# Performance work log

Measured on AMD Instinct MI355X. Metric: run time of the kernel, lower is better.

The kernel has to match this reference:

```python
import jax, jax.numpy as jnp
import numpy as np

B, N, M, U, L = 2048, 256, 128, 512, 2   # batch, memory locations, memory width, num_units, num_layers
RH, WH, SH = 2, 2, 1                      # read heads, write heads, conv_shift_range
CLIP = 20.0
HEAD_R = M + 3 + (2 * SH + 1)             # 134 = k(M)+beta+g+s(2r+1)+gamma
HEAD_W = HEAD_R + 2 * M                   # 390 = + erase(M) + add(M)


def setup_inputs():
    key = jax.random.key(0)
    ks = jax.random.split(key, 12)
    def nrm(k, shape, s=0.05):
        return jax.random.normal(k, shape, jnp.float32) * s
    return {
        "X": jax.random.normal(ks[0], (B, U), jnp.float32),
        "m0": nrm(ks[1], (1, N, M), 0.5),
        "H0": nrm(ks[2], (L, 1, U)),
        "C0": nrm(ks[3], (L, 1, U)),
        "R0": nrm(ks[4], (RH, 1, M)),
        "A0": nrm(ks[5], (RH + WH, 1, N)),
        "W_prep": nrm(ks[6], (M * RH, U)),
        "b_prep": jnp.zeros((U,), jnp.float32),
        "W_lstm": nrm(ks[7], (L, 3 * U, 4 * U)),
        "b_lstm": jnp.zeros((L, 4 * U), jnp.float32),
        "W_r": nrm(ks[8], (U, RH * HEAD_R)),
        "b_r": jnp.zeros((RH * HEAD_R,), jnp.float32),
        "W_w": nrm(ks[9], (U, WH * HEAD_W)),
        "b_w": jnp.zeros((WH * HEAD_W,), jnp.float32),
        "W_ou": nrm(ks[10], (U + RH * M, U)),
        "b_ou": jnp.zeros((U,), jnp.float32),
    }


def _addressing(k, beta, g, s, gamma, m, a_prev):
    # k [B,M], beta/g/gamma [B], s [B,2*SH+1], m [B,N,M], a_prev [B,N]
    inner = jnp.einsum('bnm,bm->bn', m, k)
    k_norm = jnp.sqrt(jnp.sum(k * k, axis=1, keepdims=True))   # [B,1]
    m_norm = jnp.sqrt(jnp.sum(m * m, axis=2))                  # [B,N]
    K = inner / (k_norm * m_norm + 1e-8)
    w_c = jax.nn.softmax(beta[:, None] * K, axis=1)            # exp/sum in source == softmax
    w_g = g[:, None] * w_c + (1.0 - g[:, None]) * a_prev
    # The stacked-slice s_matrix in the source is exactly circular convolution:
    # w_conv[i] = sum_d s_d * w_g[(i - d) mod N], d in {0..SH, -SH..-1} matching s layout.
    shifts = list(range(0, SH + 1)) + list(range(-SH, 0))
    w_conv = sum(s[:, j:j + 1] * jnp.roll(w_g, shifts[j], axis=1) for j in range(2 * SH + 1))
    w_sharp = w_conv ** gamma[:, None]
    return w_sharp / jnp.sum(w_sharp, axis=1, keepdims=True)


def reference(X, m0, H0, C0, R0, A0, W_prep, b_prep, W_lstm, b_lstm,
              W_r, b_r, W_w, b_w, W_ou, b_ou):
    b = X.shape[0]
    m = jnp.broadcast_to(m0, (b, N, M))
    R_prev = [jnp.broadcast_to(jnp.tanh(R0[i]), (b, M)) for i in range(RH)]
    A_prev = [jnp.broadcast_to(jax.nn.softmax(A0[i], axis=-1), (b, N)) for i in range(RH + WH)]

    # controller
    h = jnp.concatenate(R_prev, axis=1) @ W_prep + b_prep
    for l in range(L):
        x_in = jnp.concatenate([X, h], axis=1)                              # [B,2U]
        h_prev = jnp.broadcast_to(H0[l], (b, U))
        c_prev = jnp.broadcast_to(C0[l], (b, U))
        z = jnp.concatenate([x_in, h_prev], axis=1) @ W_lstm[l] + b_lstm[l]  # [B,4U]
        i_g, f_g, g_g, o_g = jnp.split(z, 4, axis=1)
        c = jax.nn.sigmoid(f_g) * c_prev + jax.nn.sigmoid(i_g) * jnp.tanh(g_g)
        h = jax.nn.sigmoid(o_g) * jnp.tanh(c)
    h = jnp.clip(h, -CLIP, CLIP)

    r_heads = (h @ W_r + b_r).reshape(b, RH, HEAD_R)
    w_heads = (h @ W_w + b_w).reshape(b, WH, HEAD_W)
    heads = [r_heads[:, i] for i in range(RH)] + [w_heads[:, i] for i in range(WH)]

    A_t = []
    for ii, hd in enumerate(heads):
        A_t.append(_addressing(
            k=jnp.tanh(hd[:, :M]),
            beta=jax.nn.softplus(hd[:, M]),
            g=jax.nn.sigmoid(hd[:, M + 1]),
            s=jax.nn.softmax(hd[:, M + 2:M + 2 + 2 * SH + 1], axis=-1),
            gamma=jax.nn.softplus(hd[:, M + 2 + 2 * SH + 1]),
            m=m, a_prev=A_prev[ii]))

    # reads from old memory
    R_t = [jnp.einsum('bn,bnm->bm', A_t[i], m) for i in range(RH)]

    # sequential erase/add writes
    m_t = m
    for ii in range(WH):
        w = A_t[RH + ii][:, :, None]                                  # [B,N,1]
        del_v = jax.nn.sigmoid(w_heads[:, ii, -2 * M:-M])[:, None, :]  # [B,1,M]
        add_v = jnp.tanh(w_heads[:, ii, -M:])[:, None, :]
        m_t = m_t * (1.0 - w * del_v) + w * add_v

    y = jnp.clip(jnp.concatenate([h] + R_t, axis=1) @ W_ou + b_ou, -CLIP, CLIP)
    return y, m_t
```

## Files before the change

### kernel.cpp

```cpp
#include <hip/hip_runtime.h>
#include <math.h>

static constexpr int Bn = 2048;
static constexpr int Nn = 256;
static constexpr int Mn = 128;
static constexpr int Un = 512;

static constexpr size_t OFF_MNORM = 4608;
static constexpr size_t OFF_APREV = 4864;
static constexpr size_t OFF_BIASH = 5888;
static constexpr size_t OFF_KMAT  = 16384;
static constexpr size_t OFF_HEADS = OFF_KMAT + 2097152;
static constexpr size_t OFF_AT    = OFF_HEADS + 2146304;
static constexpr size_t OFF_ERA   = OFF_AT + 1048576;
static constexpr size_t OFF_ADD   = OFF_ERA + 524288;
static constexpr size_t OFF_XHB   = OFF_ADD + 524288;
static constexpr size_t OFF_HCAT  = OFF_XHB + 1048576;
static constexpr size_t OFF_W0T   = OFF_HCAT + 1048576;
static constexpr size_t OFF_W1T   = OFF_W0T + 524288;
static constexpr size_t OFF_WRWT  = OFF_W1T + 1048576;
static constexpr size_t OFF_WCOMB = OFF_WRWT + 294912;
static constexpr size_t OFF_WR2T  = OFF_WCOMB + 262144;
static constexpr size_t OFF_M0B   = OFF_WR2T + 65536;
static constexpr size_t OFF_ZPART = OFF_M0B + 16384;
static constexpr size_t OFF_YH    = OFF_ZPART + 32768;

static constexpr int P_X0  = 0;
static constexpr int P_M0  = 512;
static constexpr int P_W0  = 528;
static constexpr int P_W1  = 1552;
static constexpr int P_WR2 = 3600;
static constexpr int P_CA  = 3728;
static constexpr int P_ZC  = 3729;
static constexpr int P_END = 3793;

static constexpr int M_L0  = 0;
static constexpr int M_ZX  = 512;
static constexpr int M_PF  = 1024;
static constexpr int M_WRr = 1056;
static constexpr int M_WRw = 1200;
static constexpr int M_WOU = 1600;
static constexpr int M_ZC1 = 1856;
static constexpr int M_END = 1920;

static constexpr int H_HD  = 0;
static constexpr int H_YH  = 288;
static constexpr int H_KM  = 416;
static constexpr int H_END = 672;

static constexpr int T_OUT = 0;
static constexpr int T_MEM = 128;
static constexpr int T_END = 384;

#define DEV __device__ __forceinline__

typedef __attribute__((ext_vector_type(8))) short bf16x8;
typedef __attribute__((ext_vector_type(4))) float f32x4;
typedef __attribute__((ext_vector_type(8))) unsigned short ushort8;
typedef unsigned int u32;

DEV float sigf(float x) { return 1.0f / (1.0f + expf(-x)); }
DEV float softplusf(float x) { return x > 20.0f ? x : log1pf(expf(x)); }
DEV unsigned short f2bf(float f) {
    unsigned u = __float_as_uint(f);
    u = (u + 0x7FFFu + ((u >> 16) & 1u)) >> 16;
    return (unsigned short)u;
}
DEV float b2f(unsigned short u) { return __uint_as_float((u32)u << 16); }
DEV void gload16(const unsigned short* g, unsigned short* l) {
    __builtin_amdgcn_global_load_lds(
        (const __attribute__((address_space(1))) u32*)g,
        (__attribute__((address_space(3))) u32*)l, 16, 0, 0);
}

DEV float blk_reduce_max(float v, float* red) {
    int tid = threadIdx.x;
    red[tid] = v; __syncthreads();
    for (int s = (int)blockDim.x >> 1; s > 0; s >>= 1) {
        if (tid < s) red[tid] = fmaxf(red[tid], red[tid + s]);
        __syncthreads();
    }
    float r = red[0]; __syncthreads();
    return r;
}
DEV float blk_reduce_sum(float v, float* red) {
    int tid = threadIdx.x;
    red[tid] = v; __syncthreads();
    for (int s = (int)blockDim.x >> 1; s > 0; s >>= 1) {
        if (tid < s) red[tid] += red[tid + s];
        __syncthreads();
    }
    float r = red[0]; __syncthreads();
    return r;
}

DEV float wv_sum(float v) {
    #pragma unroll
    for (int off = 32; off; off >>= 1) v += __shfl_xor(v, off);
    return v;
}
DEV float wv_max(float v) {
    #pragma unroll
    for (int off = 32; off; off >>= 1) v = fmaxf(v, __shfl_xor(v, off));
    return v;
}
DEV float blk_sum4(float v, float* red4) {
    v = wv_sum(v);
    int w = threadIdx.x >> 6;
    if ((threadIdx.x & 63) == 0) red4[w] = v;
    __syncthreads();
    float r = red4[0] + red4[1] + red4[2] + red4[3];
    __syncthreads();
    return r;
}
DEV float blk_max4(float v, float* red4) {
    v = wv_max(v);
    int w = threadIdx.x >> 6;
    if ((threadIdx.x & 63) == 0) red4[w] = v;
    __syncthreads();
    float r = fmaxf(fmaxf(red4[0], red4[1]), fmaxf(red4[2], red4[3]));
    __syncthreads();
    return r;
}

#define GEMM_SHARED                                                             \
    __shared__ __align__(16) unsigned short As[2][64 * 64];                     \
    __shared__ __align__(16) unsigned short Ws[2][128 * 64];

#define GEMM_REGS                                                               \
    const int tid  = threadIdx.x;                                               \
    const int lane = tid & 63;                                                  \
    const int wave = tid >> 6;                                                  \
    const int wr = wave >> 1, wc = wave & 1;                                    \
    const int ke = ((tid & 7) * 8) ^ (((tid >> 3) & 7) << 3);                   \
    const int frow = lane & 15;                                                 \
    const int fko  = (lane >> 4) * 8;                                           \
    const int fxm  = (frow & 7) << 3;                                           \
    f32x4 acc[2][4];                                                            \
    _Pragma("unroll")                                                           \
    for (int i = 0; i < 2; ++i)                                                 \
        _Pragma("unroll")                                                       \
        for (int j = 0; j < 4; ++j) acc[i][j] = (f32x4){0.f, 0.f, 0.f, 0.f};

#define GEMM_STAGE(buf, k0)                                                     \
    {                                                                           \
        _Pragma("unroll")                                                       \
        for (int q = 0; q < 2; ++q)                                             \
            gload16(A  + (size_t)(row0 + q * 32 + (tid >> 3)) * lda + (k0) + ke,\
                    &As[buf][q * 2048 + tid * 8]);                              \
        _Pragma("unroll")                                                       \
        for (int q = 0; q < 4; ++q)                                             \
            gload16(Wt + (size_t)(col0 + q * 32 + (tid >> 3)) * ldw + (k0) + ke,\
                    &Ws[buf][q * 2048 + tid * 8]);                              \
    }

#define GEMM_FRAGS_AND_MFMA(Ab, Wb)                                             \
    {                                                                           \
        bf16x8 af[2][2], wf[2][4];                                              \
        _Pragma("unroll")                                                       \
        for (int kk = 0; kk < 2; ++kk) {                                        \
            _Pragma("unroll")                                                   \
            for (int i = 0; i < 2; ++i) {                                       \
                int fr = wr * 32 + i * 16 + frow;                               \
                af[kk][i] = *(const bf16x8*)&(Ab)[fr * 64 + ((kk * 32 + fko) ^ fxm)]; \
            }                                                                   \
            _Pragma("unroll")                                                   \
            for (int j = 0; j < 4; ++j) {                                       \
                int fr = wc * 64 + j * 16 + frow;                               \
                wf[kk][j] = *(const bf16x8*)&(Wb)[fr * 64 + ((kk * 32 + fko) ^ fxm)]; \
            }                                                                   \
        }                                                                       \
        __builtin_amdgcn_s_setprio(1);                                          \
        _Pragma("unroll")                                                       \
        for (int kk = 0; kk < 2; ++kk)                                          \
            _Pragma("unroll")                                                   \
            for (int i = 0; i < 2; ++i)                                         \
                _Pragma("unroll")                                               \
                for (int j = 0; j < 4; ++j)                                     \
                    acc[i][j] = __builtin_amdgcn_mfma_f32_16x16x32_bf16(        \
                        af[kk][i], wf[kk][j], acc[i][j], 0, 0, 0);              \
        __builtin_amdgcn_s_setprio(0);                                          \
    }

#define GEMM_MAINLOOP(Kr)                                                       \
    {                                                                           \
        const int nt = (Kr) >> 6;                                               \
        int cur = 0;                                                            \
        GEMM_STAGE(0, 0);                                                       \
        for (int t = 0; t < nt; ++t) {                                          \
            if (t + 1 < nt) {                                                   \
                GEMM_STAGE(cur ^ 1, (t + 1) * 64);                              \
                asm volatile("s_waitcnt vmcnt(6)" ::: "memory");                \
            } else {                                                            \
                asm volatile("s_waitcnt vmcnt(0)" ::: "memory");                \
            }                                                                   \
            __builtin_amdgcn_sched_barrier(0);                                  \
            __builtin_amdgcn_s_barrier();                                       \
            __builtin_amdgcn_sched_barrier(0);                                  \
            GEMM_FRAGS_AND_MFMA(As[cur], Ws[cur]);                              \
            __builtin_amdgcn_sched_barrier(0);                                  \
            __builtin_amdgcn_s_barrier();                                       \
            cur ^= 1;                                                           \
        }                                                                       \
    }

#define LSTM_EPILOGUE(zc, doclip, houtp, ldhv, ZXP)                             \
    {                                                                           \
        const int uu = lane & 15;                                               \
        const int q  = (col0 >> 6) + wc;                                        \
        const int uq = q * 16 + uu;                                             \
        const float c0v = c0[(zc) * 512 + uq];                                  \
        float bg[4];                                                            \
        _Pragma("unroll")                                                       \
        for (int g = 0; g < 4; ++g) {                                           \
            int j = g * 512 + q * 16 + uu;                                      \
            float a = b_lstm[(zc) * 2048 + j];                                  \
            _Pragma("unroll")                                                   \
            for (int p = 0; p < 8; ++p)                                         \
                a += zpart[((size_t)(zc) * 8 + p) * 2048 + j];                  \
            bg[g] = a;                                                          \
        }                                                                       \
        _Pragma("unroll")                                                       \
        for (int i = 0; i < 2; ++i) {                                           \
            int rbase = row0 + wr * 32 + i * 16 + (lane >> 4) * 4;              \
            _Pragma("unroll")                                                   \
            for (int r = 0; r < 4; ++r) {                                       \
                float z0 = 0.f, z1 = 0.f, z2 = 0.f, z3 = 0.f;                   \
                if (ZXP) {                                                      \
                    const unsigned short* zr = (ZXP) +                          \
                        (size_t)(rbase + r) * 2048 + q * 64 + uu;               \
                    z0 = b2f(zr[0]);  z1 = b2f(zr[16]);                         \
                    z2 = b2f(zr[32]); z3 = b2f(zr[48]);                         \
                }                                                               \
                float ig = acc[i][0][r] + bg[0] + z0;                           \
                float fg = acc[i][1][r] + bg[1] + z1;                           \
                float gg = acc[i][2][r] + bg[2] + z2;                           \
                float og = acc[i][3][r] + bg[3] + z3;                           \
                float c = sigf(fg) * c0v + sigf(ig) * tanhf(gg);                \
                float h = sigf(og) * tanhf(c);                                  \
                if (doclip) h = fminf(fmaxf(h, -20.f), 20.f);                   \
                (houtp)[(size_t)(rbase + r) * (ldhv) + uq] = f2bf(h);           \
            }                                                                   \
        }                                                                       \
    }

DEV void dev_cvt8(const float* src, int lds, unsigned short* dst, int ldd,
                  int c8, int bloc, int tid)
{
    size_t idx = (size_t)bloc * 256 + tid;
    size_t r = idx / c8, c = (idx % c8) * 8;
    const float* s = src + r * lds + c;
    float4 v0 = *(const float4*)s;
    float4 v1 = *(const float4*)(s + 4);
    ushort8 o;
    o[0] = f2bf(v0.x); o[1] = f2bf(v0.y); o[2] = f2bf(v0.z); o[3] = f2bf(v0.w);
    o[4] = f2bf(v1.x); o[5] = f2bf(v1.y); o[6] = f2bf(v1.z); o[7] = f2bf(v1.w);
    *(ushort8*)(dst + r * ldd + c) = o;
}

DEV void dev_cvtT(const float* src, int R, int C, int lds,
                  unsigned short* dst, int ldd, int mode, int bx, int by,
                  int tid, float* t )
{
    const int x = tid & 31;
    for (int y = tid >> 5; y < 32; y += 8) {
        int r = by * 32 + y, c = bx * 32 + x;
        int scol = c;
        if (mode) scol = ((c >> 4) & 3) * 512 + (c >> 6) * 16 + (c & 15);
        t[y * 33 + x] = (r < R && c < C) ? src[(size_t)r * lds + scol] : 0.f;
    }
    __syncthreads();
    for (int y = tid >> 5; y < 32; y += 8) {
        int c = bx * 32 + y, r = by * 32 + x;
        if (c < C && r < R) dst[(size_t)c * ldd + r] = f2bf(t[x * 33 + y]);
    }
}

__global__ __launch_bounds__(256) void k_prep(
    const float* __restrict__ X, const float* __restrict__ m0,
    const float* __restrict__ H0, const float* __restrict__ R0,
    const float* __restrict__ A0, const float* __restrict__ W_prep,
    const float* __restrict__ b_prep, const float* __restrict__ W_lstm,
    const float* __restrict__ b_r, const float* __restrict__ b_w,
    const float* __restrict__ W_ou, float* __restrict__ ws)
{
    __shared__ float sh[32 * 33 + 64];
    const int bid = blockIdx.x, tid = threadIdx.x;
    unsigned short* XHB  = (unsigned short*)(ws + OFF_XHB);
    unsigned short* W0T  = (unsigned short*)(ws + OFF_W0T);
    unsigned short* W1T  = (unsigned short*)(ws + OFF_W1T);
    unsigned short* WR2T = (unsigned short*)(ws + OFF_WR2T);
    unsigned short* M0B  = (unsigned short*)(ws + OFF_M0B);

    if (bid < P_M0) {
        dev_cvt8(X, 512, XHB, 1024, 64, bid - P_X0, tid);
    } else if (bid < P_W0) {
        dev_cvt8(m0, 128, M0B, 128, 16, bid - P_M0, tid);
    } else if (bid < P_W1) {
        int s = bid - P_W0;
        dev_cvtT(W_lstm, 512, 2048, 2048, W0T, 512, 1, s & 63, s >> 6, tid, sh);
    } else if (bid < P_WR2) {
        int s = bid - P_W1;
        dev_cvtT(W_lstm + (size_t)1536 * 2048, 1024, 2048, 2048, W1T, 1024, 1,
                 s & 63, s >> 6, tid, sh);
    } else if (bid < P_CA) {
        int s = bid - P_WR2;
        dev_cvtT(W_ou + (size_t)512 * 512, 256, 512, 512, WR2T, 256, 0,
                 s & 15, s >> 4, tid, sh);
    } else if (bid < P_ZC) {
        float* red = sh;
        for (int i = 0; i < 4; ++i) {
            float v = A0[i * 256 + tid];
            float mx = blk_reduce_max(v, red);
            float e = expf(v - mx);
            float s = blk_reduce_sum(e, red);
            ws[OFF_APREV + i * 256 + tid] = e / s;
        }
        float acc = 0.f;
        for (int m = 0; m < 128; ++m) {
            float t = m0[(size_t)tid * 128 + m];
            acc = fmaf(t, t, acc);
        }
        ws[OFF_MNORM + tid] = sqrtf(acc);
        for (int j = tid; j < 1152; j += 256)
            ws[OFF_BIASH + j] = (j < 268) ? b_r[j] : (j < 1048 ? b_w[j - 268] : 0.f);
    } else {
        int sub = bid - P_ZC;
        int colb = sub & 7, up = sub >> 3;
        int j = colb * 256 + tid;
        float acc = 0.f;
        if (up < 4) {
            sh[256 + tid] = tanhf(R0[tid]);
            __syncthreads();
            if (tid < 128) {
                int u = up * 128 + tid;
                float a = b_prep[u];
                for (int k = 0; k < 256; ++k)
                    a = fmaf(sh[256 + k], W_prep[(size_t)k * 512 + u], a);
                sh[tid] = a;
            }
            __syncthreads();
            const int u0 = up * 128;
            #pragma unroll 4
            for (int t = 0; t < 128; ++t)
                acc = fmaf(sh[t], W_lstm[(size_t)(512 + u0 + t) * 2048 + j], acc);
        } else {
            const int u0 = up * 128;
            #pragma unroll 4
            for (int t = 0; t < 128; ++t)
                acc = fmaf(H0[u0 - 512 + t],
                           W_lstm[(size_t)(512 + u0 + t) * 2048 + j], acc);
        }
        (ws + OFF_ZPART)[(size_t)up * 2048 + j] = acc;
    }
}

__global__ __launch_bounds__(256) void k_mid(
    const float* __restrict__ W_lstm, const float* __restrict__ W_r,
    const float* __restrict__ W_w, const float* __restrict__ W_ou,
    const float* __restrict__ H0, const float* __restrict__ b_lstm,
    const float* __restrict__ c0, float* __restrict__ ws)
{
    GEMM_SHARED
    const int s = blockIdx.x;
    float* sh = (float*)&As[0][0];
    unsigned short* XHB   = (unsigned short*)(ws + OFF_XHB);
    unsigned short* W0T   = (unsigned short*)(ws + OFF_W0T);
    unsigned short* W1T   = (unsigned short*)(ws + OFF_W1T);
    unsigned short* WRWT  = (unsigned short*)(ws + OFF_WRWT);
    unsigned short* WCOMB = (unsigned short*)(ws + OFF_WCOMB);
    unsigned short* WR2T  = (unsigned short*)(ws + OFF_WR2T);
    unsigned short* M0B   = (unsigned short*)(ws + OFF_M0B);
    unsigned short* ZX    = (unsigned short*)(ws + OFF_KMAT);
    const float* zpart    = ws + OFF_ZPART;

    if (s < M_WRr) {
        const unsigned short *A, *Wt;
        int lda, ldw, row0, col0, Kr, mode;
        unsigned short* pCb = nullptr;
        if (s < M_ZX) {
            mode = 0;
            A = XHB;  lda = 1024; Wt = W0T; ldw = 512;
            row0 = (s & 31) * 64; col0 = (s >> 5) * 128; Kr = 512;
        } else if (s < M_PF) {
            int p = s - M_ZX;
            mode = 1;
            A = XHB;  lda = 1024; Wt = W1T; ldw = 1024;
            row0 = (p & 31) * 64; col0 = (p >> 5) * 128; Kr = 512;
        } else {
            int p = s - M_PF;
            mode = 2;
            int pz = p >> 4, py = (p >> 3) & 1, px = p & 7;
            A = WR2T + pz * 128; lda = 256; Wt = M0B; ldw = 128;
            row0 = px * 64; col0 = py * 128; Kr = 128;
            pCb = WCOMB + 512 + pz * 256;
        }
        GEMM_REGS
        GEMM_MAINLOOP(Kr)
        if (mode == 0) {
            unsigned short* hout = XHB + 512;
            const unsigned short* zxn = nullptr;
            LSTM_EPILOGUE(0, 0, hout, 1024, zxn)
        } else if (mode == 1) {
            #pragma unroll
            for (int i = 0; i < 2; ++i) {
                int m0r = row0 + wr * 32 + i * 16 + (lane >> 4) * 4;
                #pragma unroll
                for (int j = 0; j < 4; ++j) {
                    int n = col0 + wc * 64 + j * 16 + (lane & 15);
                    #pragma unroll
                    for (int r = 0; r < 4; ++r)
                        ZX[(size_t)(m0r + r) * 2048 + n] = f2bf(acc[i][j][r]);
                }
            }
        } else {
            #pragma unroll
            for (int i = 0; i < 2; ++i) {
                int m0r = row0 + wr * 32 + i * 16 + (lane >> 4) * 4;
                #pragma unroll
                for (int j = 0; j < 4; ++j) {
                    int n = col0 + wc * 64 + j * 16 + (lane & 15);
                    #pragma unroll
                    for (int r = 0; r < 4; ++r)
                        pCb[(size_t)(m0r + r) * 1024 + n] = f2bf(acc[i][j][r]);
                }
            }
        }
    } else if (s < M_WRw) {
        int s2 = s - M_WRr;
        dev_cvtT(W_r, 512, 268, 268, WRWT, 512, 0, s2 % 9, s2 / 9, threadIdx.x, sh);
    } else if (s < M_WOU) {
        int s3 = s - M_WRw;
        dev_cvtT(W_w, 512, 780, 780, WRWT + (size_t)268 * 512, 512, 0,
                 s3 % 25, s3 / 25, threadIdx.x, sh);
    } else if (s < M_ZC1) {
        int s4 = s - M_WOU;
        dev_cvtT(W_ou, 512, 512, 512, WCOMB, 1024, 0, s4 & 15, s4 >> 4,
                 threadIdx.x, sh);
    } else {
        int s5 = s - M_ZC1;
        int colb = s5 & 7, up = s5 >> 3;
        int j = colb * 256 + threadIdx.x;
        const int u0 = up * 64;
        const float* W1 = W_lstm + (size_t)1536 * 2048;
        float acc = 0.f;
        #pragma unroll 4
        for (int t = 0; t < 64; ++t)
            acc = fmaf(H0[512 + u0 + t], W1[(size_t)(1024 + u0 + t) * 2048 + j], acc);
        (ws + OFF_ZPART)[((size_t)8 + up) * 2048 + j] = acc;
    }
}

__global__ __launch_bounds__(256) void gemm_lstm(
    const unsigned short* __restrict__ A, int lda,
    const unsigned short* __restrict__ Wt, int ldw,
    const float* __restrict__ zpart, const float* __restrict__ b_lstm,
    const float* __restrict__ c0, const unsigned short* __restrict__ ZXP,
    unsigned short* __restrict__ hout)
{
    GEMM_SHARED
    const int row0 = blockIdx.x * 64;
    const int col0 = blockIdx.y * 128;
    GEMM_REGS
    GEMM_MAINLOOP(512)
    LSTM_EPILOGUE(1, 1, hout, 1024, ZXP)
}

__global__ __launch_bounds__(256) void k_hk(
    const unsigned short* __restrict__ HCAT,
    const unsigned short* __restrict__ WRWT,
    const unsigned short* __restrict__ WCOMB,
    const unsigned short* __restrict__ M0B,
    const float* __restrict__ biash,
    float* __restrict__ heads, float* __restrict__ yh,
    float* __restrict__ kmat)
{
    GEMM_SHARED
    const int s = blockIdx.x;
    if (s < H_KM) {
        const unsigned short* A = HCAT;  const int lda = 1024;
        const unsigned short* Wt;
        int ldw, row0, col0;
        if (s < H_YH) {
            Wt = WRWT; ldw = 512;
            row0 = (s & 31) * 64; col0 = (s >> 5) * 128;
        } else {
            int p = s - H_YH;
            Wt = WCOMB; ldw = 1024;
            row0 = (p & 31) * 64; col0 = (p >> 5) * 128;
        }
        GEMM_REGS
        GEMM_MAINLOOP(512)
        if (s < H_YH) {
            #pragma unroll
            for (int i = 0; i < 2; ++i) {
                int m0r = row0 + wr * 32 + i * 16 + (lane >> 4) * 4;
                #pragma unroll
                for (int j = 0; j < 4; ++j) {
                    int n = col0 + wc * 64 + j * 16 + (lane & 15);
                    if (n >= 1048) continue;
                    float bv = biash[n];
                    #pragma unroll
                    for (int r = 0; r < 4; ++r)
                        heads[(size_t)(m0r + r) * 1048 + n] = acc[i][j][r] + bv;
                }
            }
        } else {
            #pragma unroll
            for (int i = 0; i < 2; ++i) {
                int m0r = row0 + wr * 32 + i * 16 + (lane >> 4) * 4;
                #pragma unroll
                for (int j = 0; j < 4; ++j) {
                    int n = col0 + wc * 64 + j * 16 + (lane & 15);
                    #pragma unroll
                    for (int r = 0; r < 4; ++r)
                        yh[(size_t)(m0r + r) * 512 + n] = acc[i][j][r];
                }
            }
        }
    } else {
        int p = s - H_KM;
        const int ih = p >> 6;
        const int bt = (p >> 1) & 31;
        const int nt = p & 1;
        const int cb = (ih < 2) ? ih * 134 : 268 + (ih - 2) * 390;
        const unsigned short* A  = HCAT;          const int lda = 1024;
        const unsigned short* Wt = WRWT + (size_t)cb * 512;  const int ldw = 512;
        const int row0 = bt * 64;
        const int col0 = 0;
        GEMM_REGS
        GEMM_MAINLOOP(512)

        #pragma unroll
        for (int i = 0; i < 2; ++i) {
            int rloc = wr * 32 + i * 16 + (lane >> 4) * 4;
            #pragma unroll
            for (int j = 0; j < 4; ++j) {
                int kloc = wc * 64 + j * 16 + (lane & 15);
                float bk = biash[cb + kloc];
                int buf = kloc >> 6;
                int lg = (kloc >> 3) & 7, off = kloc & 7;
                #pragma unroll
                for (int r = 0; r < 4; ++r) {
                    int row = rloc + r;
                    As[buf][row * 64 + (((lg ^ (row & 7)) << 3) | off)] =
                        f2bf(tanhf(acc[i][j][r] + bk));
                }
            }
        }
        #pragma unroll
        for (int i = 0; i < 2; ++i)
            #pragma unroll
            for (int j = 0; j < 4; ++j) acc[i][j] = (f32x4){0.f, 0.f, 0.f, 0.f};
        const int nb0 = nt * 128;
        #pragma unroll
        for (int kt = 0; kt < 2; ++kt)
            #pragma unroll
            for (int q = 0; q < 4; ++q)
                gload16(M0B + (size_t)(nb0 + q * 32 + (tid >> 3)) * 128 + kt * 64 + ke,
                        &Ws[kt][q * 2048 + tid * 8]);
        __syncthreads();
        GEMM_FRAGS_AND_MFMA(As[0], Ws[0]);
        GEMM_FRAGS_AND_MFMA(As[1], Ws[1]);
        #pragma unroll
        for (int i = 0; i < 2; ++i) {
            int rloc = wr * 32 + i * 16 + (lane >> 4) * 4;
            #pragma unroll
            for (int j = 0; j < 4; ++j) {
                int n = nb0 + wc * 64 + j * 16 + (lane & 15);
                #pragma unroll
                for (int r = 0; r < 4; ++r)
                    kmat[((size_t)ih * 2048 + row0 + rloc + r) * 256 + n] =
                        acc[i][j][r];
            }
        }
    }
}

__global__ __launch_bounds__(256) void k_addr(
    const float* __restrict__ heads, const float* __restrict__ kmat,
    const float* __restrict__ mnorm, const float* __restrict__ aprev,
    float* __restrict__ at, unsigned short* __restrict__ hcat,
    float* __restrict__ era, float* __restrict__ addv)
{
    __shared__ float red4[4];
    __shared__ float wgs[256];
    __shared__ float sc[6];
    const int b = blockIdx.x, i = blockIdx.y, tid = threadIdx.x;
    const int cb = (i < 2) ? i * 134 : 268 + (i - 2) * 390;
    const float* hd = heads + (size_t)b * 1048 + cb;
    float kv = (tid < 128) ? tanhf(hd[tid]) : 0.f;
    float kn = sqrtf(blk_sum4(kv * kv, red4));
    if (i >= 2 && tid < 128) {
        era [((size_t)b * 2 + (i - 2)) * 128 + tid] = sigf(hd[134 + tid]);
        addv[((size_t)b * 2 + (i - 2)) * 128 + tid] = tanhf(hd[262 + tid]);
    }
    if (tid == 0) {
        sc[0] = softplusf(hd[128]);
        sc[1] = sigf(hd[129]);
        float v0 = hd[130], v1 = hd[131], v2 = hd[132];
        float mx = fmaxf(v0, fmaxf(v1, v2));
        float e0 = expf(v0 - mx), e1 = expf(v1 - mx), e2 = expf(v2 - mx);
        float ssum = e0 + e1 + e2;
        sc[2] = e0 / ssum; sc[3] = e1 / ssum; sc[4] = e2 / ssum;
        sc[5] = softplusf(hd[133]);
    }
    __syncthreads();
    const float beta = sc[0], g = sc[1], s0 = sc[2], s1 = sc[3], s2 = sc[4],
                gamma = sc[5];
    float inner = kmat[((size_t)i * 2048 + b) * 256 + tid];
    float K = inner / (kn * mnorm[tid] + 1e-8f);
    float x = beta * K;
    float mx = blk_max4(x, red4);
    float e = expf(x - mx);
    float se = blk_sum4(e, red4);
    float wc = e / se;
    float wg = g * wc + (1.f - g) * aprev[i * 256 + tid];
    wgs[tid] = wg;
    __syncthreads();
    float wconv = s0 * wg + s1 * wgs[(tid + 255) & 255] + s2 * wgs[(tid + 1) & 255];
    float wsh = powf(wconv, gamma);
    float ssum = blk_sum4(wsh, red4);
    float w = wsh / ssum;
    if (i < 2) hcat[(size_t)b * 1024 + 512 + i * 256 + tid] = f2bf(w);
    else       at[((size_t)(i - 2) * Bn + b) * 256 + tid] = w;
}

__global__ __launch_bounds__(256) void k_tail(
    const unsigned short* __restrict__ HCAT,
    const unsigned short* __restrict__ WCOMB,
    const float* __restrict__ yh, const float* __restrict__ b_ou,
    const float* __restrict__ m0, const float* __restrict__ at,
    const float* __restrict__ era, const float* __restrict__ addv,
    float* __restrict__ out)
{
    GEMM_SHARED
    const int s = blockIdx.x;
    if (s < T_MEM) {
        const unsigned short* A  = HCAT + 512;        const int lda = 1024;
        const unsigned short* Wt = WCOMB + 512;       const int ldw = 1024;
        const int row0 = (s & 31) * 64;
        const int col0 = (s >> 5) * 128;
        GEMM_REGS
        GEMM_MAINLOOP(512)
        #pragma unroll
        for (int i = 0; i < 2; ++i) {
            int m0r = row0 + wr * 32 + i * 16 + (lane >> 4) * 4;
            #pragma unroll
            for (int j = 0; j < 4; ++j) {
                int n = col0 + wc * 64 + j * 16 + (lane & 15);
                if (n >= 512) continue;
                float bv = b_ou[n];
                #pragma unroll
                for (int r = 0; r < 4; ++r) {
                    float v = acc[i][j][r] + bv + yh[(size_t)(m0r + r) * 512 + n];
                    out[(size_t)(m0r + r) * 512 + n] = fminf(fmaxf(v, -20.f), 20.f);
                }
            }
        }
    } else {
        const int tid = threadIdx.x;
        const int b0 = (s - T_MEM) * 8;
        float (*at_s)[8][256] = (float(*)[8][256])(&As[0][0]);
        float (*er_s)[8][128] = (float(*)[8][128])(&Ws[0][0]);
        float (*ad_s)[8][128] = (float(*)[8][128])(&Ws[0][4096]);
        for (int t = tid; t < 1024; t += 256) {
            int i = t >> 9, rem = t & 511;
            int bb = rem >> 6, n4 = rem & 63;
            ((float4*)&at_s[i][bb][0])[n4] =
                ((const float4*)(at + ((size_t)i * Bn + b0 + bb) * 256))[n4];
        }
        for (int t = tid; t < 512; t += 256) {
            int i = t >> 8, rem = t & 255;
            int bb = rem >> 5, m4 = rem & 31;
            ((float4*)&er_s[i][bb][0])[m4] =
                ((const float4*)(era + ((size_t)(b0 + bb) * 2 + i) * 128))[m4];
            ((float4*)&ad_s[i][bb][0])[m4] =
                ((const float4*)(addv + ((size_t)(b0 + bb) * 2 + i) * 128))[m4];
        }
        __syncthreads();
        const float4* m0v = (const float4*)m0;
        float4* outv = (float4*)(out + (size_t)Bn * Un);
        for (int pos = tid; pos < 8192; pos += 256) {
            int mq = pos & 31, n = pos >> 5;
            float4 t0 = m0v[pos];
            #pragma unroll
            for (int bb = 0; bb < 8; ++bb) {
                float w0 = at_s[0][bb][n], w1 = at_s[1][bb][n];
                float4 e0 = *(const float4*)&er_s[0][bb][mq * 4];
                float4 a0 = *(const float4*)&ad_s[0][bb][mq * 4];
                float4 e1 = *(const float4*)&er_s[1][bb][mq * 4];
                float4 a1 = *(const float4*)&ad_s[1][bb][mq * 4];
                float4 t = t0;
#define UPD(c) { t.c = t.c * (1.f - w0 * e0.c) + w0 * a0.c; \
                 t.c = t.c * (1.f - w1 * e1.c) + w1 * a1.c; }
                UPD(x) UPD(y) UPD(z) UPD(w)
#undef UPD
                __builtin_nontemporal_store(*(f32x4*)&t,
                    (f32x4*)&outv[(size_t)(b0 + bb) * 8192 + pos]);
            }
        }
    }
}

extern "C" void kernel_launch(void* const* d_in, const int* in_sizes, int n_in,
                              void* d_out, int out_size, void* d_ws, size_t ws_size,
                              hipStream_t stream)
{
    const float* X      = (const float*)d_in[0];
    const float* m0     = (const float*)d_in[1];
    const float* H0     = (const float*)d_in[2];
    const float* C0     = (const float*)d_in[3];
    const float* R0     = (const float*)d_in[4];
    const float* A0     = (const float*)d_in[5];
    const float* W_prep = (const float*)d_in[6];
    const float* b_prep = (const float*)d_in[7];
    const float* W_lstm = (const float*)d_in[8];
    const float* b_lstm = (const float*)d_in[9];
    const float* W_r    = (const float*)d_in[10];
    const float* b_r    = (const float*)d_in[11];
    const float* W_w    = (const float*)d_in[12];
    const float* b_w    = (const float*)d_in[13];
    const float* W_ou   = (const float*)d_in[14];
    const float* b_ou   = (const float*)d_in[15];
    float* ws  = (float*)d_ws;
    float* out = (float*)d_out;

    unsigned short* XHB   = (unsigned short*)(ws + OFF_XHB);
    unsigned short* HCAT  = (unsigned short*)(ws + OFF_HCAT);
    unsigned short* W1T   = (unsigned short*)(ws + OFF_W1T);
    unsigned short* WRWT  = (unsigned short*)(ws + OFF_WRWT);
    unsigned short* WCOMB = (unsigned short*)(ws + OFF_WCOMB);
    unsigned short* M0B   = (unsigned short*)(ws + OFF_M0B);
    unsigned short* ZX    = (unsigned short*)(ws + OFF_KMAT);

    k_prep<<<P_END, 256, 0, stream>>>(
        X, m0, H0, R0, A0, W_prep, b_prep, W_lstm, b_r, b_w, W_ou, ws);

    k_mid<<<M_END, 256, 0, stream>>>(
        W_lstm, W_r, W_w, W_ou, H0, b_lstm, C0, ws);

    gemm_lstm<<<dim3(32, 16), 256, 0, stream>>>(
        XHB + 512, 1024, W1T + 512, 1024, ws + OFF_ZPART, b_lstm, C0, ZX, HCAT);

    k_hk<<<H_END, 256, 0, stream>>>(
        HCAT, WRWT, WCOMB, M0B, ws + OFF_BIASH, ws + OFF_HEADS, ws + OFF_YH,
        ws + OFF_KMAT);

    k_addr<<<dim3(Bn, 4), 256, 0, stream>>>(
        ws + OFF_HEADS, ws + OFF_KMAT, ws + OFF_MNORM, ws + OFF_APREV,
        ws + OFF_AT, HCAT, ws + OFF_ERA, ws + OFF_ADD);

    k_tail<<<T_END, 256, 0, stream>>>(
        HCAT, WCOMB, ws + OFF_YH, b_ou, m0, ws + OFF_AT, ws + OFF_ERA,
        ws + OFF_ADD, out);
}
```

Before: 167.1 us.

## Fuse write-head addressing into memory-update tail blocks

Write-head addressing (weights, erase and add vectors) is now computed inside the k_tail memory-update blocks and kept in shared memory, instead of being produced by k_addr and written to global buffers. k_addr now launches only for the two read heads. This removes the global round trip of the at/era/add buffers and halves the k_addr grid. In exchange, each tail block runs 16 serial addressing passes, each with several block-wide barriers, before its update loop, which may lengthen the critical path of those blocks.

```diff
diff --git a/kernel.cpp b/kernel.cpp
--- a/kernel.cpp
+++ b/kernel.cpp
@@ -11,10 +11,7 @@
 static constexpr size_t OFF_BIASH = 5888;
 static constexpr size_t OFF_KMAT  = 16384;
 static constexpr size_t OFF_HEADS = OFF_KMAT + 2097152;
-static constexpr size_t OFF_AT    = OFF_HEADS + 2146304;
-static constexpr size_t OFF_ERA   = OFF_AT + 1048576;
-static constexpr size_t OFF_ADD   = OFF_ERA + 524288;
-static constexpr size_t OFF_XHB   = OFF_ADD + 524288;
+static constexpr size_t OFF_XHB   = OFF_HEADS + 2146304;
 static constexpr size_t OFF_HCAT  = OFF_XHB + 1048576;
 static constexpr size_t OFF_W0T   = OFF_HCAT + 1048576;
 static constexpr size_t OFF_W1T   = OFF_W0T + 524288;
@@ -580,21 +577,15 @@
 __global__ __launch_bounds__(256) void k_addr(
     const float* __restrict__ heads, const float* __restrict__ kmat,
     const float* __restrict__ mnorm, const float* __restrict__ aprev,
-    float* __restrict__ at, unsigned short* __restrict__ hcat,
-    float* __restrict__ era, float* __restrict__ addv)
+    unsigned short* __restrict__ hcat)
 {
     __shared__ float red4[4];
     __shared__ float wgs[256];
     __shared__ float sc[6];
     const int b = blockIdx.x, i = blockIdx.y, tid = threadIdx.x;
-    const int cb = (i < 2) ? i * 134 : 268 + (i - 2) * 390;
-    const float* hd = heads + (size_t)b * 1048 + cb;
+    const float* hd = heads + (size_t)b * 1048 + i * 134;
     float kv = (tid < 128) ? tanhf(hd[tid]) : 0.f;
     float kn = sqrtf(blk_sum4(kv * kv, red4));
-    if (i >= 2 && tid < 128) {
-        era [((size_t)b * 2 + (i - 2)) * 128 + tid] = sigf(hd[134 + tid]);
-        addv[((size_t)b * 2 + (i - 2)) * 128 + tid] = tanhf(hd[262 + tid]);
-    }
     if (tid == 0) {
         sc[0] = softplusf(hd[128]);
         sc[1] = sigf(hd[129]);
@@ -621,18 +612,16 @@
     float wconv = s0 * wg + s1 * wgs[(tid + 255) & 255] + s2 * wgs[(tid + 1) & 255];
     float wsh = powf(wconv, gamma);
     float ssum = blk_sum4(wsh, red4);
-    float w = wsh / ssum;
-    if (i < 2) hcat[(size_t)b * 1024 + 512 + i * 256 + tid] = f2bf(w);
-    else       at[((size_t)(i - 2) * Bn + b) * 256 + tid] = w;
+    hcat[(size_t)b * 1024 + 512 + i * 256 + tid] = f2bf(wsh / ssum);
 }
 
 __global__ __launch_bounds__(256) void k_tail(
     const unsigned short* __restrict__ HCAT,
     const unsigned short* __restrict__ WCOMB,
     const float* __restrict__ yh, const float* __restrict__ b_ou,
-    const float* __restrict__ m0, const float* __restrict__ at,
-    const float* __restrict__ era, const float* __restrict__ addv,
-    float* __restrict__ out)
+    const float* __restrict__ m0, const float* __restrict__ heads,
+    const float* __restrict__ kmat, const float* __restrict__ mnorm,
+    const float* __restrict__ aprev, float* __restrict__ out)
 {
     GEMM_SHARED
     const int s = blockIdx.x;
@@ -664,21 +653,52 @@
         float (*at_s)[8][256] = (float(*)[8][256])(&As[0][0]);
         float (*er_s)[8][128] = (float(*)[8][128])(&Ws[0][0]);
         float (*ad_s)[8][128] = (float(*)[8][128])(&Ws[0][4096]);
-        for (int t = tid; t < 1024; t += 256) {
-            int i = t >> 9, rem = t & 511;
-            int bb = rem >> 6, n4 = rem & 63;
-            ((float4*)&at_s[i][bb][0])[n4] =
-                ((const float4*)(at + ((size_t)i * Bn + b0 + bb) * 256))[n4];
-        }
-        for (int t = tid; t < 512; t += 256) {
-            int i = t >> 8, rem = t & 255;
-            int bb = rem >> 5, m4 = rem & 31;
-            ((float4*)&er_s[i][bb][0])[m4] =
-                ((const float4*)(era + ((size_t)(b0 + bb) * 2 + i) * 128))[m4];
-            ((float4*)&ad_s[i][bb][0])[m4] =
-                ((const float4*)(addv + ((size_t)(b0 + bb) * 2 + i) * 128))[m4];
-        }
-        __syncthreads();
+        float* xtra = (float*)&Ws[1][0];
+        float* wgs  = xtra;
+        float* red4 = xtra + 256;
+        float* sc   = xtra + 260;
+
+        for (int t16 = 0; t16 < 16; ++t16) {
+            const int ii = t16 >> 3, bb = t16 & 7;
+            const int b = b0 + bb;
+            const float* hd = heads + (size_t)b * 1048 + 268 + ii * 390;
+            float kv = (tid < 128) ? tanhf(hd[tid]) : 0.f;
+            float kn = sqrtf(blk_sum4(kv * kv, red4));
+            if (tid < 128) {
+                er_s[ii][bb][tid] = sigf(hd[134 + tid]);
+                ad_s[ii][bb][tid] = tanhf(hd[262 + tid]);
+            }
+            if (tid == 0) {
+                sc[0] = softplusf(hd[128]);
+                sc[1] = sigf(hd[129]);
+                float v0 = hd[130], v1 = hd[131], v2 = hd[132];
+                float mx = fmaxf(v0, fmaxf(v1, v2));
+                float e0 = expf(v0 - mx), e1 = expf(v1 - mx), e2 = expf(v2 - mx);
+                float ssum = e0 + e1 + e2;
+                sc[2] = e0 / ssum; sc[3] = e1 / ssum; sc[4] = e2 / ssum;
+                sc[5] = softplusf(hd[133]);
+            }
+            __syncthreads();
+            const float beta = sc[0], g = sc[1], s0 = sc[2], s1 = sc[3],
+                        s2 = sc[4], gamma = sc[5];
+            float inner = kmat[((size_t)(2 + ii) * 2048 + b) * 256 + tid];
+            float K = inner / (kn * mnorm[tid] + 1e-8f);
+            float x = beta * K;
+            float mx = blk_max4(x, red4);
+            float e = expf(x - mx);
+            float se = blk_sum4(e, red4);
+            float wcv = e / se;
+            float wg = g * wcv + (1.f - g) * aprev[(2 + ii) * 256 + tid];
+            wgs[tid] = wg;
+            __syncthreads();
+            float wconv = s0 * wg + s1 * wgs[(tid + 255) & 255]
+                        + s2 * wgs[(tid + 1) & 255];
+            float wsh = powf(wconv, gamma);
+            float ssum = blk_sum4(wsh, red4);
+            at_s[ii][bb][tid] = wsh / ssum;
+            __syncthreads();
+        }
+
         const float4* m0v = (const float4*)m0;
         float4* outv = (float4*)(out + (size_t)Bn * Un);
         for (int pos = tid; pos < 8192; pos += 256) {
@@ -747,11 +767,10 @@
         HCAT, WRWT, WCOMB, M0B, ws + OFF_BIASH, ws + OFF_HEADS, ws + OFF_YH,
         ws + OFF_KMAT);
 
-    k_addr<<<dim3(Bn, 4), 256, 0, stream>>>(
-        ws + OFF_HEADS, ws + OFF_KMAT, ws + OFF_MNORM, ws + OFF_APREV,
-        ws + OFF_AT, HCAT, ws + OFF_ERA, ws + OFF_ADD);
+    k_addr<<<dim3(Bn, 2), 256, 0, stream>>>(
+        ws + OFF_HEADS, ws + OFF_KMAT, ws + OFF_MNORM, ws + OFF_APREV, HCAT);
 
     k_tail<<<T_END, 256, 0, stream>>>(
-        HCAT, WCOMB, ws + OFF_YH, b_ou, m0, ws + OFF_AT, ws + OFF_ERA,
-        ws + OFF_ADD, out);
-}
+        HCAT, WCOMB, ws + OFF_YH, b_ou, m0, ws + OFF_HEADS, ws + OFF_KMAT,
+        ws + OFF_MNORM, ws + OFF_APREV, out);
+}
```

Measured after the change: 210.0 us. +25.6%, slower.
